# Kernel optimization log

Measured on AMD Instinct MI355X. Metric: run time of the kernel, lower is better.

## Reference

```python
import jax, jax.numpy as jnp
import numpy as np

N = 500_000          # total nodes in the batched graph
B = 4096             # number of graphs
D_NODE = 256         # node_feature_size
D_GRAPH = 256        # graph_feature_size
D_LOGIT = 10         # logit_mlp_sizes[0]


def setup_inputs() -> dict:
    key = jax.random.key(0)
    ks = jax.random.split(key, 12)
    s = 0.05
    node_feats = jax.random.normal(ks[0], (N, D_NODE), dtype=jnp.float32)
    graph_feats = jax.random.normal(ks[1], (B, D_GRAPH), dtype=jnp.float32)
    segment_ids = jnp.sort(jax.random.randint(ks[2], (N,), 0, B)).astype(jnp.int64)
    # message MLP: Linear(node -> graph)
    W_msg = jax.random.normal(ks[3], (D_GRAPH, D_NODE), dtype=jnp.float32) * s
    b_msg = jnp.zeros((D_GRAPH,), dtype=jnp.float32)
    # logit MLP: Linear(node+graph -> 10) -> LeakyReLU -> Linear(10 -> 1) -> LeakyReLU
    W_l1 = jax.random.normal(ks[4], (D_LOGIT, D_NODE + D_GRAPH), dtype=jnp.float32) * s
    b_l1 = jnp.zeros((D_LOGIT,), dtype=jnp.float32)
    W_l2 = jax.random.normal(ks[5], (1, D_LOGIT), dtype=jnp.float32) * s
    b_l2 = jnp.zeros((1,), dtype=jnp.float32)
    # GRUCell(graph, graph): torch layout [3H, H] gates ordered (r, z, n)
    W_ih = jax.random.normal(ks[6], (3 * D_GRAPH, D_GRAPH), dtype=jnp.float32) * s
    W_hh = jax.random.normal(ks[7], (3 * D_GRAPH, D_GRAPH), dtype=jnp.float32) * s
    b_ih = jnp.zeros((3 * D_GRAPH,), dtype=jnp.float32)
    b_hh = jnp.zeros((3 * D_GRAPH,), dtype=jnp.float32)
    return dict(node_feats=node_feats, graph_feats=graph_feats, segment_ids=segment_ids,
                W_msg=W_msg, b_msg=b_msg, W_l1=W_l1, b_l1=b_l1, W_l2=W_l2, b_l2=b_l2,
                W_ih=W_ih, W_hh=W_hh, b_ih=b_ih, b_hh=b_hh)


def _segment_softmax(logits, seg, num_segments):
    # logits: [N, 1]; stable softmax per graph
    m = jax.ops.segment_max(logits, seg, num_segments=num_segments)      # [B,1]
    m = jnp.where(jnp.isfinite(m), m, 0.0)                               # empty segments
    ex = jnp.exp(logits - m[seg])                                        # [N,1]
    denom = jax.ops.segment_sum(ex, seg, num_segments=num_segments)      # [B,1]
    return ex / jnp.maximum(denom[seg], 1e-30)


def reference(node_feats, graph_feats, segment_ids, W_msg, b_msg,
              W_l1, b_l1, W_l2, b_l2, W_ih, W_hh, b_ih, b_hh):
    seg = segment_ids.astype(jnp.int32)
    num_graphs = graph_feats.shape[0]

    # (1) node logits: MLP on [broadcast(relu(graph_feats)), node_feats]
    g_bcast = jax.nn.relu(graph_feats)[seg]                              # [N, Dg]
    x = jnp.concatenate([g_bcast, node_feats], axis=1)                   # [N, Dg+Dn]
    h = jax.nn.leaky_relu(x @ W_l1.T + b_l1)                             # [N, 10]
    logits = jax.nn.leaky_relu(h @ W_l2.T + b_l2)                        # [N, 1]

    # (2) per-graph softmax over nodes
    alpha = _segment_softmax(logits, seg, num_graphs)                    # [N, 1]

    # (3) messages
    m = node_feats @ W_msg.T + b_msg                                     # [N, Dg]

    # (4) context: weighted segment sum
    context = jax.ops.segment_sum(alpha * m, seg, num_segments=num_graphs)  # [B, Dg]

    # (5) GRU update (torch GRUCell, gate order r,z,n)
    H = graph_feats.shape[1]
    gi = context @ W_ih.T + b_ih                                         # [B, 3H]
    gh = graph_feats @ W_hh.T + b_hh                                     # [B, 3H]
    i_r, i_z, i_n = gi[:, :H], gi[:, H:2*H], gi[:, 2*H:]
    h_r, h_z, h_n = gh[:, :H], gh[:, H:2*H], gh[:, 2*H:]
    r = jax.nn.sigmoid(i_r + h_r)
    z = jax.nn.sigmoid(i_z + h_z)
    n = jnp.tanh(i_n + r * h_n)
    return (1.0 - z) * n + z * graph_feats
```

## Files before the change

kernel.cpp:

```cpp
#include <hip/hip_runtime.h>
#include <math.h>

#define DG 256
#define DL 10
#define TN 32
#define NBLK 512

__device__ __forceinline__ float leaky(float x) { return x > 0.f ? x : 0.01f * x; }
__device__ __forceinline__ float sigmoidf(float x) { return 1.f / (1.f + expf(-x)); }

__global__ void k_glog(const float* __restrict__ gf, const float* __restrict__ W_l1,
                       const float* __restrict__ b_l1, float* __restrict__ glog,
                       float* __restrict__ pooled, float* __restrict__ denom) {
  int b = blockIdx.x;
  int l = threadIdx.x;
  float4 g4 = *(const float4*)(gf + (size_t)b * DG + 4 * l);
  g4.x = fmaxf(g4.x, 0.f); g4.y = fmaxf(g4.y, 0.f);
  g4.z = fmaxf(g4.z, 0.f); g4.w = fmaxf(g4.w, 0.f);
  float p[DL];
#pragma unroll
  for (int j = 0; j < DL; ++j) {
    float4 w4 = *(const float4*)(W_l1 + (size_t)j * 512 + 4 * l);
    p[j] = g4.x * w4.x + g4.y * w4.y + g4.z * w4.z + g4.w * w4.w;
  }
#pragma unroll
  for (int m = 32; m >= 1; m >>= 1) {
#pragma unroll
    for (int j = 0; j < DL; ++j) p[j] += __shfl_xor(p[j], m);
  }
  *(float4*)(pooled + (size_t)b * 256 + 4 * l) = make_float4(0.f, 0.f, 0.f, 0.f);
  if (l == 0) {
#pragma unroll
    for (int j = 0; j < DL; ++j) glog[b * 12 + j] = p[j] + b_l1[j];
    glog[b * 12 + 10] = 0.f;
    glog[b * 12 + 11] = 0.f;
    denom[b] = 0.f;
  }
}

__global__ void k_transpose3(const float* __restrict__ A, const float* __restrict__ Bm,
                             const float* __restrict__ C, float* __restrict__ AT,
                             float* __restrict__ BT, float* __restrict__ CT) {
  int idx = blockIdx.x * blockDim.x + threadIdx.x;
  if (idx < 65536) {
    int r = idx >> 8, c = idx & 255;
    AT[c * 256 + r] = A[idx];
  } else if (idx < 262144) {
    int i = idx - 65536;
    int r = i >> 8, c = i & 255;
    BT[c * 768 + r] = Bm[i];
  } else {
    int i = idx - 262144;
    int r = i >> 8, c = i & 255;
    CT[c * 768 + r] = C[i];
  }
}

__global__ __launch_bounds__(256) void k_fused(
    const float* __restrict__ nf, const int* __restrict__ seg,
    const float* __restrict__ W_l1, const float* __restrict__ glog,
    const float* __restrict__ W_l2, const float* __restrict__ b_l2_p,
    float* __restrict__ pooled, float* __restrict__ denom, int N) {
  __shared__ __align__(16) float xs[TN * 256];
  __shared__ __align__(16) float pq[TN * 84];
  __shared__ __align__(16) float wl[DL * 256];
  __shared__ float sex[TN];
  __shared__ int gsg[TN];

  const int t = threadIdx.x;
  const int sstride = (seg[N - 1] == 0) ? 2 : 1;

  for (int i = t; i < DL * 64; i += 256) {
    int j = i >> 6, c4 = i & 63;
    *(float4*)(wl + j * 256 + 4 * c4) =
        *(const float4*)(W_l1 + (size_t)j * 512 + 256 + 4 * c4);
  }
  float wl2[DL];
#pragma unroll
  for (int j = 0; j < DL; ++j) wl2[j] = W_l2[j];
  const float bl2 = b_l2_p[0];

  const int ntiles = (N + TN - 1) / TN;
  const int n = t & 31;
  const int q = t >> 5;
  const int sw = n & 7;

  float4 R[8];
  int tile = blockIdx.x;
  {
    const int n0 = tile * TN;
#pragma unroll
    for (int i = 0; i < 8; ++i) {
      int f4i = i * 256 + t;
      int row = f4i >> 6, col = f4i & 63;
      int gr = min(n0 + row, N - 1);
      R[i] = *(const float4*)(nf + ((size_t)gr << 8) + 4 * (col ^ (row & 7)));
    }
  }

  for (; tile < ntiles; tile += NBLK) {
    const int n0 = tile * TN;
    __syncthreads();
#pragma unroll
    for (int i = 0; i < 8; ++i) {
      int f4i = i * 256 + t;
      int row = f4i >> 6, col = f4i & 63;
      *(float4*)(xs + (row << 8) + 4 * col) = R[i];
    }
    if (t < TN) {
      int gr = min(n0 + t, N - 1);
      gsg[t] = seg[(size_t)gr * sstride];
    }
    __syncthreads();

    {
      int tn2 = tile + NBLK;
      if (tn2 < ntiles) {
        const int m0 = tn2 * TN;
#pragma unroll
        for (int i = 0; i < 8; ++i) {
          int f4i = i * 256 + t;
          int row = f4i >> 6, col = f4i & 63;
          int gr = min(m0 + row, N - 1);
          R[i] = *(const float4*)(nf + ((size_t)gr << 8) + 4 * (col ^ (row & 7)));
        }
      }
    }

    float p[DL];
#pragma unroll
    for (int j = 0; j < DL; ++j) p[j] = 0.f;
#pragma unroll
    for (int i = 0; i < 8; ++i) {
      const float4 x4 = *(const float4*)(xs + (n << 8) + 4 * (((q << 3) + i) ^ sw));
      const float* wq = wl + (q << 5) + 4 * i;
#pragma unroll
      for (int j = 0; j < DL; ++j) {
        const float4 w4 = *(const float4*)(wq + j * 256);
        p[j] += x4.x * w4.x + x4.y * w4.y + x4.z * w4.z + x4.w * w4.w;
      }
    }
#pragma unroll
    for (int j = 0; j < DL; ++j) pq[n * 84 + 8 * j + q] = p[j];
    __syncthreads();

    if (t < TN) {
      const int g = gsg[t];
      const float* gp = glog + g * 12;
      float gl[12];
      *(float4*)(gl + 0) = *(const float4*)(gp + 0);
      *(float4*)(gl + 4) = *(const float4*)(gp + 4);
      *(float4*)(gl + 8) = *(const float4*)(gp + 8);
      float acc = bl2;
#pragma unroll
      for (int j = 0; j < DL; ++j) {
        const float4 a = *(const float4*)(pq + t * 84 + 8 * j);
        const float4 b4 = *(const float4*)(pq + t * 84 + 8 * j + 4);
        float s = ((a.x + a.y) + (a.z + a.w)) + ((b4.x + b4.y) + (b4.z + b4.w)) + gl[j];
        acc += wl2[j] * leaky(s);
      }
      float lg = leaky(acc);
      sex[t] = (n0 + t < N) ? expf(lg) : 0.f;
    }
    __syncthreads();

    {
      float acc = 0.f, accd = 0.f;
      int cur = gsg[0];
#pragma unroll 4
      for (int nn = 0; nn < TN; ++nn) {
        int g = gsg[nn];
        if (g != cur) {
          atomicAdd(pooled + ((size_t)cur << 8) + t, acc);
          if (t == 0) atomicAdd(denom + cur, accd);
          acc = 0.f; accd = 0.f; cur = g;
        }
        float e = sex[nn];
        acc += e * xs[(nn << 8) + (t ^ ((nn & 7) << 2))];
        accd += e;
      }
      atomicAdd(pooled + ((size_t)cur << 8) + t, acc);
      if (t == 0) atomicAdd(denom + cur, accd);
    }
  }
}

__global__ __launch_bounds__(256) void k_gru(
    const float* __restrict__ pooled, const float* __restrict__ denom,
    const float* __restrict__ gf, const float* __restrict__ WmsgT,
    const float* __restrict__ b_msg, const float* __restrict__ WihT,
    const float* __restrict__ WhhT, const float* __restrict__ b_ih,
    const float* __restrict__ b_hh, float* __restrict__ out) {
  __shared__ float pool_s[8][256];
  __shared__ float gf_s[8][256];
  __shared__ float ctx_s[8][256];

  const int t = threadIdx.x;
  const int b0 = blockIdx.x * 8;
  const int dt = t & 63;
  const int g0 = (t >> 6) * 2;

#pragma unroll
  for (int g = 0; g < 8; ++g) {
    float dn = fmaxf(denom[b0 + g], 1e-30f);
    pool_s[g][t] = pooled[(size_t)(b0 + g) * 256 + t] / dn;
    gf_s[g][t] = gf[(size_t)(b0 + g) * 256 + t];
  }
  __syncthreads();

  {
    float acc[2][4] = {{0.f, 0.f, 0.f, 0.f}, {0.f, 0.f, 0.f, 0.f}};
#pragma unroll 4
    for (int k = 0; k < 256; ++k) {
      float4 w = *(const float4*)(WmsgT + (size_t)k * 256 + 4 * dt);
#pragma unroll
      for (int gi = 0; gi < 2; ++gi) {
        float pv = pool_s[g0 + gi][k];
        acc[gi][0] += pv * w.x; acc[gi][1] += pv * w.y;
        acc[gi][2] += pv * w.z; acc[gi][3] += pv * w.w;
      }
    }
    float4 bm = *(const float4*)(b_msg + 4 * dt);
#pragma unroll
    for (int gi = 0; gi < 2; ++gi) {
      ctx_s[g0 + gi][4 * dt + 0] = acc[gi][0] + bm.x;
      ctx_s[g0 + gi][4 * dt + 1] = acc[gi][1] + bm.y;
      ctx_s[g0 + gi][4 * dt + 2] = acc[gi][2] + bm.z;
      ctx_s[g0 + gi][4 * dt + 3] = acc[gi][3] + bm.w;
    }
  }
  __syncthreads();

  float r[2][4], z[2][4];

#pragma unroll
  for (int s = 0; s < 2; ++s) {
    float ai[2][4] = {{0.f, 0.f, 0.f, 0.f}, {0.f, 0.f, 0.f, 0.f}};
    float ah[2][4] = {{0.f, 0.f, 0.f, 0.f}, {0.f, 0.f, 0.f, 0.f}};
#pragma unroll 4
    for (int k = 0; k < 256; ++k) {
      float4 wi = *(const float4*)(WihT + (size_t)k * 768 + s * 256 + 4 * dt);
      float4 wh = *(const float4*)(WhhT + (size_t)k * 768 + s * 256 + 4 * dt);
#pragma unroll
      for (int gi = 0; gi < 2; ++gi) {
        float c = ctx_s[g0 + gi][k];
        float h = gf_s[g0 + gi][k];
        ai[gi][0] += c * wi.x; ai[gi][1] += c * wi.y; ai[gi][2] += c * wi.z; ai[gi][3] += c * wi.w;
        ah[gi][0] += h * wh.x; ah[gi][1] += h * wh.y; ah[gi][2] += h * wh.z; ah[gi][3] += h * wh.w;
      }
    }
    float4 bi = *(const float4*)(b_ih + s * 256 + 4 * dt);
    float4 bh = *(const float4*)(b_hh + s * 256 + 4 * dt);
#pragma unroll
    for (int gi = 0; gi < 2; ++gi) {
      float v0 = sigmoidf(ai[gi][0] + bi.x + ah[gi][0] + bh.x);
      float v1 = sigmoidf(ai[gi][1] + bi.y + ah[gi][1] + bh.y);
      float v2 = sigmoidf(ai[gi][2] + bi.z + ah[gi][2] + bh.z);
      float v3 = sigmoidf(ai[gi][3] + bi.w + ah[gi][3] + bh.w);
      if (s == 0) { r[gi][0] = v0; r[gi][1] = v1; r[gi][2] = v2; r[gi][3] = v3; }
      else        { z[gi][0] = v0; z[gi][1] = v1; z[gi][2] = v2; z[gi][3] = v3; }
    }
  }

  {
    float ai[2][4] = {{0.f, 0.f, 0.f, 0.f}, {0.f, 0.f, 0.f, 0.f}};
    float ah[2][4] = {{0.f, 0.f, 0.f, 0.f}, {0.f, 0.f, 0.f, 0.f}};
#pragma unroll 4
    for (int k = 0; k < 256; ++k) {
      float4 wi = *(const float4*)(WihT + (size_t)k * 768 + 512 + 4 * dt);
      float4 wh = *(const float4*)(WhhT + (size_t)k * 768 + 512 + 4 * dt);
#pragma unroll
      for (int gi = 0; gi < 2; ++gi) {
        float c = ctx_s[g0 + gi][k];
        float h = gf_s[g0 + gi][k];
        ai[gi][0] += c * wi.x; ai[gi][1] += c * wi.y; ai[gi][2] += c * wi.z; ai[gi][3] += c * wi.w;
        ah[gi][0] += h * wh.x; ah[gi][1] += h * wh.y; ah[gi][2] += h * wh.z; ah[gi][3] += h * wh.w;
      }
    }
    float4 bi = *(const float4*)(b_ih + 512 + 4 * dt);
    float4 bh = *(const float4*)(b_hh + 512 + 4 * dt);
#pragma unroll
    for (int gi = 0; gi < 2; ++gi) {
      float4 o;
      float hf0 = gf_s[g0 + gi][4 * dt + 0];
      float hf1 = gf_s[g0 + gi][4 * dt + 1];
      float hf2 = gf_s[g0 + gi][4 * dt + 2];
      float hf3 = gf_s[g0 + gi][4 * dt + 3];
      float n0 = tanhf(ai[gi][0] + bi.x + r[gi][0] * (ah[gi][0] + bh.x));
      float n1 = tanhf(ai[gi][1] + bi.y + r[gi][1] * (ah[gi][1] + bh.y));
      float n2 = tanhf(ai[gi][2] + bi.z + r[gi][2] * (ah[gi][2] + bh.z));
      float n3 = tanhf(ai[gi][3] + bi.w + r[gi][3] * (ah[gi][3] + bh.w));
      o.x = (1.f - z[gi][0]) * n0 + z[gi][0] * hf0;
      o.y = (1.f - z[gi][1]) * n1 + z[gi][1] * hf1;
      o.z = (1.f - z[gi][2]) * n2 + z[gi][2] * hf2;
      o.w = (1.f - z[gi][3]) * n3 + z[gi][3] * hf3;
      *(float4*)(out + (size_t)(b0 + g0 + gi) * 256 + 4 * dt) = o;
    }
  }
}

extern "C" void kernel_launch(void* const* d_in, const int* in_sizes, int n_in,
                              void* d_out, int out_size, void* d_ws, size_t ws_size,
                              hipStream_t stream) {
  const float* nf    = (const float*)d_in[0];
  const float* gf    = (const float*)d_in[1];
  const int*   seg   = (const int*)d_in[2];
  const float* W_msg = (const float*)d_in[3];
  const float* b_msg = (const float*)d_in[4];
  const float* W_l1  = (const float*)d_in[5];
  const float* b_l1  = (const float*)d_in[6];
  const float* W_l2  = (const float*)d_in[7];
  const float* b_l2  = (const float*)d_in[8];
  const float* W_ih  = (const float*)d_in[9];
  const float* W_hh  = (const float*)d_in[10];
  const float* b_ih  = (const float*)d_in[11];
  const float* b_hh  = (const float*)d_in[12];
  float* out = (float*)d_out;

  const int N = in_sizes[0] / 256;
  const int B = in_sizes[1] / 256;

  size_t off = 0;
  char* base = (char*)d_ws;
  auto alloc = [&](size_t bytes) -> void* {
    void* p = base + off;
    off += (bytes + 255) & ~(size_t)255;
    return p;
  };
  float* glog   = (float*)alloc((size_t)B * 12 * sizeof(float));
  float* WmsgT  = (float*)alloc((size_t)256 * 256 * sizeof(float));
  float* WihT   = (float*)alloc((size_t)768 * 256 * sizeof(float));
  float* WhhT   = (float*)alloc((size_t)768 * 256 * sizeof(float));
  float* pooled = (float*)alloc((size_t)B * 256 * sizeof(float));
  float* denom  = (float*)alloc((size_t)B * sizeof(float));

  k_glog<<<B, 64, 0, stream>>>(gf, W_l1, b_l1, glog, pooled, denom);
  k_transpose3<<<(65536 + 2 * 196608 + 255) / 256, 256, 0, stream>>>(
      W_msg, W_ih, W_hh, WmsgT, WihT, WhhT);

  const int ntiles = (N + TN - 1) / TN;
  const int nblk = ntiles < NBLK ? ntiles : NBLK;
  k_fused<<<nblk, 256, 0, stream>>>(nf, seg, W_l1, glog, W_l2, b_l2, pooled, denom, N);

  k_gru<<<B / 8, 256, 0, stream>>>(pooled, denom, gf, WmsgT, b_msg, WihT, WhhT,
                                   b_ih, b_hh, out);
}
```

Measured before the change: 1.073 ms.

## Use direct global-to-LDS loads, contiguous tile ranges, and cross-tile segment accumulation

The fused node kernel now loads node-feature tiles straight into LDS with global_load_lds instead of staging them through registers, and gives each block a contiguous range of tiles rather than a strided one. Per-graph partial sums are carried across tiles in registers and flushed with shuffle reductions and atomics only when the segment changes, using a ballot mask of segment starts. The W_l1 LDS staging is removed in favour of direct global reads, and the grid grows from 512 to 768 blocks. The intent is fewer atomics and less register/VGPR pressure on this bandwidth-bound pass. The cost is losing the explicit register-prefetch overlap of the next tile, which the direct-to-LDS path is expected to make up for.

```diff
diff --git a/kernel.cpp b/kernel.cpp
--- a/kernel.cpp
+++ b/kernel.cpp
@@ -1,13 +1,20 @@
 #include <hip/hip_runtime.h>
 #include <math.h>
+#include <stdint.h>
 
 #define DG 256
 #define DL 10
 #define TN 32
-#define NBLK 512
+#define NBLK 768
 
 __device__ __forceinline__ float leaky(float x) { return x > 0.f ? x : 0.01f * x; }
 __device__ __forceinline__ float sigmoidf(float x) { return 1.f / (1.f + expf(-x)); }
+
+__device__ __forceinline__ void gll16(const float* src, float* dst) {
+  typedef __attribute__((address_space(1))) const unsigned int gu32;
+  typedef __attribute__((address_space(3))) unsigned int lu32;
+  __builtin_amdgcn_global_load_lds((gu32*)src, (lu32*)dst, 16, 0, 0);
+}
 
 __global__ void k_glog(const float* __restrict__ gf, const float* __restrict__ W_l1,
                        const float* __restrict__ b_l1, float* __restrict__ glog,
@@ -63,125 +70,154 @@
     float* __restrict__ pooled, float* __restrict__ denom, int N) {
   __shared__ __align__(16) float xs[TN * 256];
   __shared__ __align__(16) float pq[TN * 84];
-  __shared__ __align__(16) float wl[DL * 256];
   __shared__ float sex[TN];
   __shared__ int gsg[TN];
+  __shared__ unsigned smask;
 
   const int t = threadIdx.x;
+  const int l = t & 63;
+  const int w = t >> 6;
   const int sstride = (seg[N - 1] == 0) ? 2 : 1;
 
-  for (int i = t; i < DL * 64; i += 256) {
-    int j = i >> 6, c4 = i & 63;
-    *(float4*)(wl + j * 256 + 4 * c4) =
-        *(const float4*)(W_l1 + (size_t)j * 512 + 256 + 4 * c4);
-  }
+  const int ntiles = (N + TN - 1) / TN;
+  const int q0 = ntiles / NBLK, r0 = ntiles % NBLK;
+  const int bid = blockIdx.x;
+  const int tile_lo = bid * q0 + (bid < r0 ? bid : r0);
+  const int tile_hi = tile_lo + q0 + (bid < r0 ? 1 : 0);
+
+  const int nB = t & 31, qB = t >> 5;
+  const int swB = nB & 7;
+  const int dq = (w << 4) + (l & 15);
+  const int ns = l >> 4;
+  const bool dlane = (w == 0) && ((l & 15) == 0);
+
   float wl2[DL];
 #pragma unroll
   for (int j = 0; j < DL; ++j) wl2[j] = W_l2[j];
   const float bl2 = b_l2_p[0];
 
-  const int ntiles = (N + TN - 1) / TN;
-  const int n = t & 31;
-  const int q = t >> 5;
-  const int sw = n & 7;
-
-  float4 R[8];
-  int tile = blockIdx.x;
-  {
-    const int n0 = tile * TN;
-#pragma unroll
-    for (int i = 0; i < 8; ++i) {
-      int f4i = i * 256 + t;
-      int row = f4i >> 6, col = f4i & 63;
-      int gr = min(n0 + row, N - 1);
-      R[i] = *(const float4*)(nf + ((size_t)gr << 8) + 4 * (col ^ (row & 7)));
-    }
-  }
-
-  for (; tile < ntiles; tile += NBLK) {
+  float ax = 0.f, ay = 0.f, az = 0.f, aw = 0.f, ad = 0.f;
+  int cur = -1;
+
+  for (int tile = tile_lo; tile < tile_hi; ++tile) {
     const int n0 = tile * TN;
     __syncthreads();
-#pragma unroll
-    for (int i = 0; i < 8; ++i) {
-      int f4i = i * 256 + t;
-      int row = f4i >> 6, col = f4i & 63;
-      *(float4*)(xs + (row << 8) + 4 * col) = R[i];
+
+#pragma unroll
+    for (int rr = 0; rr < 8; ++rr) {
+      const int r = (w << 3) + rr;
+      int gr = n0 + r; if (gr > N - 1) gr = N - 1;
+      const float* src = nf + ((size_t)gr << 8) + 4 * (l ^ (r & 7));
+      gll16(src, xs + (r << 8));
     }
     if (t < TN) {
-      int gr = min(n0 + t, N - 1);
+      int gr = n0 + t; if (gr > N - 1) gr = N - 1;
       gsg[t] = seg[(size_t)gr * sstride];
     }
     __syncthreads();
 
     {
-      int tn2 = tile + NBLK;
-      if (tn2 < ntiles) {
-        const int m0 = tn2 * TN;
-#pragma unroll
-        for (int i = 0; i < 8; ++i) {
-          int f4i = i * 256 + t;
-          int row = f4i >> 6, col = f4i & 63;
-          int gr = min(m0 + row, N - 1);
-          R[i] = *(const float4*)(nf + ((size_t)gr << 8) + 4 * (col ^ (row & 7)));
+      float p[DL];
+#pragma unroll
+      for (int j = 0; j < DL; ++j) p[j] = 0.f;
+      const float* wbase = W_l1 + 256 + (qB << 5);
+#pragma unroll 2
+      for (int i = 0; i < 8; ++i) {
+        const float4 x4 =
+            *(const float4*)(xs + (nB << 8) + 4 * (((qB << 3) + i) ^ swB));
+#pragma unroll
+        for (int j = 0; j < DL; ++j) {
+          const float4 w4 = *(const float4*)(wbase + (size_t)j * 512 + 4 * i);
+          p[j] += x4.x * w4.x + x4.y * w4.y + x4.z * w4.z + x4.w * w4.w;
         }
       }
-    }
-
-    float p[DL];
-#pragma unroll
-    for (int j = 0; j < DL; ++j) p[j] = 0.f;
-#pragma unroll
-    for (int i = 0; i < 8; ++i) {
-      const float4 x4 = *(const float4*)(xs + (n << 8) + 4 * (((q << 3) + i) ^ sw));
-      const float* wq = wl + (q << 5) + 4 * i;
-#pragma unroll
-      for (int j = 0; j < DL; ++j) {
-        const float4 w4 = *(const float4*)(wq + j * 256);
-        p[j] += x4.x * w4.x + x4.y * w4.y + x4.z * w4.z + x4.w * w4.w;
-      }
-    }
-#pragma unroll
-    for (int j = 0; j < DL; ++j) pq[n * 84 + 8 * j + q] = p[j];
+#pragma unroll
+      for (int j = 0; j < DL; ++j) pq[nB * 84 + 8 * j + qB] = p[j];
+    }
     __syncthreads();
 
-    if (t < TN) {
-      const int g = gsg[t];
-      const float* gp = glog + g * 12;
-      float gl[12];
-      *(float4*)(gl + 0) = *(const float4*)(gp + 0);
-      *(float4*)(gl + 4) = *(const float4*)(gp + 4);
-      *(float4*)(gl + 8) = *(const float4*)(gp + 8);
-      float acc = bl2;
-#pragma unroll
-      for (int j = 0; j < DL; ++j) {
-        const float4 a = *(const float4*)(pq + t * 84 + 8 * j);
-        const float4 b4 = *(const float4*)(pq + t * 84 + 8 * j + 4);
-        float s = ((a.x + a.y) + (a.z + a.w)) + ((b4.x + b4.y) + (b4.z + b4.w)) + gl[j];
-        acc += wl2[j] * leaky(s);
-      }
-      float lg = leaky(acc);
-      sex[t] = (n0 + t < N) ? expf(lg) : 0.f;
+    if (t < 64) {
+      bool strt = false;
+      if (t < TN) {
+        const int g = gsg[t];
+        const float* gp = glog + g * 12;
+        float gl[12];
+        *(float4*)(gl + 0) = *(const float4*)(gp + 0);
+        *(float4*)(gl + 4) = *(const float4*)(gp + 4);
+        *(float4*)(gl + 8) = *(const float4*)(gp + 8);
+        float acc = bl2;
+#pragma unroll
+        for (int j = 0; j < DL; ++j) {
+          const float4 a = *(const float4*)(pq + t * 84 + 8 * j);
+          const float4 b4 = *(const float4*)(pq + t * 84 + 8 * j + 4);
+          float s = ((a.x + a.y) + (a.z + a.w)) + ((b4.x + b4.y) + (b4.z + b4.w)) + gl[j];
+          acc += wl2[j] * leaky(s);
+        }
+        float lg = leaky(acc);
+        sex[t] = (n0 + t < N) ? expf(lg) : 0.f;
+        strt = (t == 0) || (gsg[t] != gsg[t - 1]);
+      }
+      unsigned long long bm = __ballot(strt);
+      if (t == 0) smask = (unsigned)bm;
     }
     __syncthreads();
 
     {
-      float acc = 0.f, accd = 0.f;
-      int cur = gsg[0];
-#pragma unroll 4
-      for (int nn = 0; nn < TN; ++nn) {
-        int g = gsg[nn];
+      const unsigned m = smask;
+      int a = 0;
+      while (a < TN) {
+        const int g = gsg[a];
+        const unsigned rest = (a < 31) ? (m >> (a + 1)) : 0u;
+        const int b = rest ? (a + __ffs(rest)) : TN;
         if (g != cur) {
-          atomicAdd(pooled + ((size_t)cur << 8) + t, acc);
-          if (t == 0) atomicAdd(denom + cur, accd);
-          acc = 0.f; accd = 0.f; cur = g;
+          if (cur >= 0) {
+            float vx = ax, vy = ay, vz = az, vw = aw, vd = ad;
+            vx += __shfl_xor(vx, 16); vy += __shfl_xor(vy, 16);
+            vz += __shfl_xor(vz, 16); vw += __shfl_xor(vw, 16);
+            vd += __shfl_xor(vd, 16);
+            vx += __shfl_xor(vx, 32); vy += __shfl_xor(vy, 32);
+            vz += __shfl_xor(vz, 32); vw += __shfl_xor(vw, 32);
+            vd += __shfl_xor(vd, 32);
+            if ((l & 48) == 0) {
+              float* p = pooled + ((size_t)cur << 8) + 4 * dq;
+              atomicAdd(p + 0, vx); atomicAdd(p + 1, vy);
+              atomicAdd(p + 2, vz); atomicAdd(p + 3, vw);
+            }
+            if (t == 0) atomicAdd(denom + cur, vd);
+          }
+          ax = ay = az = aw = ad = 0.f;
+          cur = g;
         }
-        float e = sex[nn];
-        acc += e * xs[(nn << 8) + (t ^ ((nn & 7) << 2))];
-        accd += e;
-      }
-      atomicAdd(pooled + ((size_t)cur << 8) + t, acc);
-      if (t == 0) atomicAdd(denom + cur, accd);
-    }
+#pragma unroll
+        for (int k = 0; k < 8; ++k) {
+          const int node = (ns << 3) + k;
+          const bool act = (node >= a) && (node < b);
+          float e = sex[node];
+          e = act ? e : 0.f;
+          const float4 x4 =
+              *(const float4*)(xs + (node << 8) + 4 * (dq ^ (node & 7)));
+          ax += e * x4.x; ay += e * x4.y; az += e * x4.z; aw += e * x4.w;
+          ad += dlane ? e : 0.f;
+        }
+        a = b;
+      }
+    }
+  }
+
+  if (cur >= 0) {
+    float vx = ax, vy = ay, vz = az, vw = aw, vd = ad;
+    vx += __shfl_xor(vx, 16); vy += __shfl_xor(vy, 16);
+    vz += __shfl_xor(vz, 16); vw += __shfl_xor(vw, 16);
+    vd += __shfl_xor(vd, 16);
+    vx += __shfl_xor(vx, 32); vy += __shfl_xor(vy, 32);
+    vz += __shfl_xor(vz, 32); vw += __shfl_xor(vw, 32);
+    vd += __shfl_xor(vd, 32);
+    if ((l & 48) == 0) {
+      float* p = pooled + ((size_t)cur << 8) + 4 * dq;
+      atomicAdd(p + 0, vx); atomicAdd(p + 1, vy);
+      atomicAdd(p + 2, vz); atomicAdd(p + 3, vw);
+    }
+    if (t == 0) atomicAdd(denom + cur, vd);
   }
 }
 
@@ -212,12 +248,12 @@
     float acc[2][4] = {{0.f, 0.f, 0.f, 0.f}, {0.f, 0.f, 0.f, 0.f}};
 #pragma unroll 4
     for (int k = 0; k < 256; ++k) {
-      float4 w = *(const float4*)(WmsgT + (size_t)k * 256 + 4 * dt);
+      float4 wv = *(const float4*)(WmsgT + (size_t)k * 256 + 4 * dt);
 #pragma unroll
       for (int gi = 0; gi < 2; ++gi) {
         float pv = pool_s[g0 + gi][k];
-        acc[gi][0] += pv * w.x; acc[gi][1] += pv * w.y;
-        acc[gi][2] += pv * w.z; acc[gi][3] += pv * w.w;
+        acc[gi][0] += pv * wv.x; acc[gi][1] += pv * wv.y;
+        acc[gi][2] += pv * wv.z; acc[gi][3] += pv * wv.w;
       }
     }
     float4 bm = *(const float4*)(b_msg + 4 * dt);
@@ -338,9 +374,8 @@
   k_transpose3<<<(65536 + 2 * 196608 + 255) / 256, 256, 0, stream>>>(
       W_msg, W_ih, W_hh, WmsgT, WihT, WhhT);
 
-  const int ntiles = (N + TN - 1) / TN;
-  const int nblk = ntiles < NBLK ? ntiles : NBLK;
-  k_fused<<<nblk, 256, 0, stream>>>(nf, seg, W_l1, glog, W_l2, b_l2, pooled, denom, N);
+  k_fused<<<NBLK, 256, 0, stream>>>(nf, seg, W_l1, glog, W_l2, b_l2, pooled,
+                                    denom, N);
 
   k_gru<<<B / 8, 256, 0, stream>>>(pooled, denom, gf, WmsgT, b_msg, WihT, WhhT,
                                    b_ih, b_hh, out);
```

After: 1.011 ms. 5.8% less time.
